# Performance work log

Hardware: AMD Instinct MI355X
Metric: run time of the kernel (lower is better)

The kernel has to match this reference:

```python
import jax, jax.numpy as jnp
import numpy as np

N = 100000
E = 1600000
IN_DIM = 128
HID = 64
EPS = 1e-5


def setup_inputs() -> dict:
    key = jax.random.key(0)
    ks = jax.random.split(key, 16)
    inp = {
        "x": jax.random.normal(ks[0], (N, IN_DIM), dtype=jnp.float32),
        "edge_index": jax.random.randint(ks[1], (2, E), 0, N, dtype=jnp.int64),
    }
    dims = [(HID, IN_DIM), (HID, HID), (HID, HID)]
    for i, (o, c) in enumerate(dims):
        inp[f"W{i}"] = jax.random.normal(ks[2 + 4 * i], (o, c), dtype=jnp.float32) / np.sqrt(c)
        inp[f"b{i}"] = jnp.zeros((o,), dtype=jnp.float32)
        inp[f"g{i}"] = jnp.ones((o,), dtype=jnp.float32)
        inp[f"be{i}"] = jnp.zeros((o,), dtype=jnp.float32)
    return inp


def _gcn_layer(x, W, b, src, dst, norm):
    # PyG GCNConv: linear first, then normalized sum aggregation, then bias
    h = x @ W.T                                  # [N, out]
    msg = h[src] * norm[:, None]                 # [E+N, out] gather (memory-bound)
    agg = jax.ops.segment_sum(msg, dst, num_segments=N)
    return agg + b


def _batchnorm(h, g, be):
    mean = jnp.mean(h, axis=0)
    var = jnp.mean((h - mean) ** 2, axis=0)      # biased var (training-mode BN)
    return (h - mean) * jax.lax.rsqrt(var + EPS) * g + be


def reference(x, edge_index, W0, b0, g0, be0, W1, b1, g1, be1, W2, b2, g2, be2):
    # add self loops (GCNConv default)
    loops = jnp.arange(N, dtype=edge_index.dtype)
    src = jnp.concatenate([edge_index[0], loops])
    dst = jnp.concatenate([edge_index[1], loops])
    # symmetric normalization: deg^{-1/2}[src] * deg^{-1/2}[dst]
    deg = jax.ops.segment_sum(jnp.ones_like(dst, dtype=x.dtype), dst, num_segments=N)
    dis = jax.lax.rsqrt(jnp.maximum(deg, 1.0))
    norm = dis[src] * dis[dst]

    params = [(W0, b0, g0, be0), (W1, b1, g1, be1), (W2, b2, g2, be2)]
    for W, b, g, be in params:
        h = _gcn_layer(x, W, b, src, dst, norm)
        h = _batchnorm(h, g, be)
        h = jax.nn.relu(h)
        x = x + h if h.shape == x.shape else h   # residual from layer 2 on
    return x
```

## Files before the change

### kernel.cpp

```cpp
#include <hip/hip_runtime.h>
#include <math.h>

#define NN 100000
#define NE 1600000
#define EPS_BN 1e-5f
#define NB 1000
#define BSZ 100
#define PCHUNK 8192

__device__ __forceinline__ unsigned bf16r(float x) {
  unsigned u = __float_as_uint(x);
  return (u + 0x7FFFu + ((u >> 16) & 1u)) >> 16;
}
__device__ __forceinline__ float bf16lo(unsigned w) { return __uint_as_float(w << 16); }
__device__ __forceinline__ float bf16hi(unsigned w) { return __uint_as_float(w & 0xFFFF0000u); }

__global__ void detect_kernel(const int* __restrict__ ei32, int* __restrict__ flag) {
  __shared__ int red[256];
  int t = threadIdx.x;
  int acc = 0;
#pragma unroll
  for (int k = 0; k < 4; ++k) acc |= ei32[2 * (t * 4 + k) + 1];
  red[t] = acc;
  __syncthreads();
  for (int off = 128; off > 0; off >>= 1) {
    if (t < off) red[t] |= red[t + off];
    __syncthreads();
  }
  if (t == 0) *flag = (red[0] == 0) ? 1 : 0;
}

__device__ __forceinline__ int edge_at(const void* ei, long long idx, int is64) {
  if (is64) return (int)((const long long*)ei)[idx];
  return ((const int*)ei)[idx];
}

__global__ __launch_bounds__(256) void bhist_kernel(const void* __restrict__ ei,
                                                    const int* __restrict__ flag,
                                                    int* __restrict__ bucket_cnt) {
  __shared__ int h[NB];
  int is64 = *flag;
  int t = threadIdx.x;
  for (int k = t; k < NB; k += 256) h[k] = 0;
  __syncthreads();
  for (int e = blockIdx.x * 256 + t; e < NE; e += gridDim.x * 256) {
    int d = edge_at(ei, (long long)NE + e, is64);
    atomicAdd(&h[d / BSZ], 1);
  }
  __syncthreads();
  for (int k = t; k < NB; k += 256) {
    int v = h[k];
    if (v) atomicAdd(&bucket_cnt[k], v);
  }
}

__global__ __launch_bounds__(1024) void bscan_kernel(const int* __restrict__ bucket_cnt,
                                                     int* __restrict__ bucket_base,
                                                     int* __restrict__ bucket_put,
                                                     int* __restrict__ row_start) {
  __shared__ int sh[1024];
  int t = threadIdx.x;
  int v = (t < NB) ? bucket_cnt[t] : 0;
  sh[t] = v;
  __syncthreads();
  for (int off = 1; off < 1024; off <<= 1) {
    int u = (t >= off) ? sh[t - off] : 0;
    __syncthreads();
    sh[t] += u;
    __syncthreads();
  }
  if (t < NB) {
    int b = sh[t] - v;
    bucket_base[t] = b;
    bucket_put[t] = b;
  }
  if (t == 0) row_start[NN] = NE;
}

__global__ __launch_bounds__(256) void bplace_kernel(const void* __restrict__ ei,
                                                     const int* __restrict__ flag,
                                                     int* __restrict__ bucket_put,
                                                     unsigned* __restrict__ staging) {
  __shared__ int hist[NB];
  __shared__ int base[NB];
  int is64 = *flag;
  int t = threadIdx.x;
  long long e0 = (long long)blockIdx.x * PCHUNK;
  int n = (int)min((long long)PCHUNK, (long long)NE - e0);
  for (int k = t; k < NB; k += 256) hist[k] = 0;
  __syncthreads();
  for (int k = t; k < n; k += 256) {
    int d = edge_at(ei, (long long)NE + e0 + k, is64);
    atomicAdd(&hist[d / BSZ], 1);
  }
  __syncthreads();
  for (int k = t; k < NB; k += 256) {
    int c = hist[k];
    base[k] = c ? atomicAdd(&bucket_put[k], c) : 0;
    hist[k] = 0;
  }
  __syncthreads();
  for (int k = t; k < n; k += 256) {
    int s = edge_at(ei, e0 + k, is64);
    int d = edge_at(ei, (long long)NE + e0 + k, is64);
    int b = d / BSZ;
    int p = base[b] + atomicAdd(&hist[b], 1);
    staging[p] = ((unsigned)s << 7) | (unsigned)(d - b * BSZ);
  }
}

__global__ __launch_bounds__(256) void bbuild_kernel(const unsigned* __restrict__ staging,
                                                     const int* __restrict__ bucket_base,
                                                     const int* __restrict__ bucket_cnt,
                                                     int* __restrict__ row_start,
                                                     float* __restrict__ dis,
                                                     int* __restrict__ csr_src) {
  __shared__ int deg[BSZ];
  __shared__ int excl[128];
  __shared__ int cur[BSZ];
  int b = blockIdx.x;
  int t = threadIdx.x;
  int base = bucket_base[b], cnt = bucket_cnt[b];
  for (int k = t; k < BSZ; k += 256) {
    deg[k] = 0;
    cur[k] = 0;
  }
  __syncthreads();
  for (int e = t; e < cnt; e += 256) {
    unsigned w = staging[base + e];
    atomicAdd(&deg[w & 127], 1);
  }
  __syncthreads();
  if (t < 128) excl[t] = (t < BSZ) ? deg[t] : 0;
  __syncthreads();
  for (int off = 1; off < 128; off <<= 1) {
    int u = 0;
    if (t < 128 && t >= off) u = excl[t - off];
    __syncthreads();
    if (t < 128) excl[t] += u;
    __syncthreads();
  }
  if (t < BSZ) {
    int ex = excl[t] - deg[t];
    row_start[b * BSZ + t] = base + ex;
    dis[b * BSZ + t] = rsqrtf((float)(deg[t] + 1));
    excl[t] = ex;
  }
  __syncthreads();
  for (int e = t; e < cnt; e += 256) {
    unsigned w = staging[base + e];
    int dl = w & 127;
    int p = base + excl[dl] + atomicAdd(&cur[dl], 1);
    csr_src[p] = (int)(w >> 7);
  }
}

__device__ __forceinline__ void bn_prologue(const float* __restrict__ stats,
                                            const float* __restrict__ g,
                                            const float* __restrict__ be, float* scb,
                                            float* shb, int t) {
  if (t < 64) {
    float m = stats[t] / (float)NN;
    float v = stats[64 + t] / (float)NN - m * m;
    float sc = g[t] * rsqrtf(fmaxf(v, 0.f) + EPS_BN);
    scb[t] = sc;
    shb[t] = be[t] - m * sc;
  }
}

template <int K>
__global__ __launch_bounds__(256) void gemm_kernel(const float* __restrict__ x,
                                                   const float* __restrict__ Wm,
                                                   const float* __restrict__ dis,
                                                   unsigned* __restrict__ h16) {
  constexpr int KC = K / 4;
  __shared__ float4 ws4[64 * KC];
  __shared__ float4 xs4[64 * KC];
  int t = threadIdx.x;
  int row0 = blockIdx.x * 64;
  const float4* W4 = (const float4*)Wm;
  for (int idx = t; idx < 64 * KC; idx += 256) {
    int j = idx / KC, kc = idx % KC;
    ws4[j * KC + (kc ^ (j & 7))] = W4[idx];
  }
  const float4* x4 = (const float4*)x;
  for (int idx = t; idx < 64 * KC; idx += 256) {
    int r = idx / KC, kc = idx % KC;
    int row = row0 + r;
    float4 v = make_float4(0.f, 0.f, 0.f, 0.f);
    if (row < NN) v = x4[(size_t)row * KC + kc];
    xs4[r * KC + kc] = v;
  }
  __syncthreads();
  int j = t & 63, wv = t >> 6;
  float acc[16];
#pragma unroll
  for (int r = 0; r < 16; ++r) acc[r] = 0.f;
  for (int kc = 0; kc < KC; ++kc) {
    float4 w = ws4[j * KC + (kc ^ (j & 7))];
#pragma unroll
    for (int r = 0; r < 16; ++r) {
      float4 xv = xs4[(wv * 16 + r) * KC + kc];
      acc[r] += w.x * xv.x + w.y * xv.y + w.z * xv.z + w.w * xv.w;
    }
  }
#pragma unroll
  for (int r = 0; r < 16; ++r) {
    int row = row0 + wv * 16 + r;
    float di = (row < NN) ? dis[row] : 0.f;
    float a = acc[r] * di;
    float part = __shfl_xor(a, 1, 64);
    if (row < NN && !(j & 1)) {
      h16[(size_t)row * 32 + (j >> 1)] = bf16r(a) | (bf16r(part) << 16);
    }
  }
}

template <bool RES>
__global__ __launch_bounds__(256) void gemmF_kernel(
    const float4* __restrict__ aggp, const float* __restrict__ stats,
    const float* __restrict__ g, const float* __restrict__ be,
    const float4* __restrict__ xres, float4* __restrict__ xout,
    const float* __restrict__ Wm, const float* __restrict__ dis,
    unsigned* __restrict__ h16) {
  constexpr int KC = 16;
  __shared__ float4 ws4[64 * KC];
  __shared__ float4 xs4[64 * KC];
  __shared__ float scb[64], shb[64];
  int t = threadIdx.x;
  int row0 = blockIdx.x * 64;
  bn_prologue(stats, g, be, scb, shb, t);
  const float4* W4 = (const float4*)Wm;
  for (int idx = t; idx < 64 * KC; idx += 256) {
    int j = idx / KC, kc = idx % KC;
    ws4[j * KC + (kc ^ (j & 7))] = W4[idx];
  }
  __syncthreads();
  for (int idx = t; idx < 64 * KC; idx += 256) {
    int r = idx / KC, kc = idx % KC;
    int row = row0 + r;
    float4 y = make_float4(0.f, 0.f, 0.f, 0.f);
    if (row < NN) {
      float4 a = aggp[(size_t)row * KC + kc];
      int f = kc * 4;
      y.x = fmaxf(fmaf(a.x, scb[f], shb[f]), 0.f);
      y.y = fmaxf(fmaf(a.y, scb[f + 1], shb[f + 1]), 0.f);
      y.z = fmaxf(fmaf(a.z, scb[f + 2], shb[f + 2]), 0.f);
      y.w = fmaxf(fmaf(a.w, scb[f + 3], shb[f + 3]), 0.f);
      if (RES) {
        float4 xr = xres[(size_t)row * KC + kc];
        y.x += xr.x;
        y.y += xr.y;
        y.z += xr.z;
        y.w += xr.w;
      }
      xout[(size_t)row * KC + kc] = y;
    }
    xs4[r * KC + kc] = y;
  }
  __syncthreads();
  int j = t & 63, wv = t >> 6;
  float acc[16];
#pragma unroll
  for (int r = 0; r < 16; ++r) acc[r] = 0.f;
  for (int kc = 0; kc < KC; ++kc) {
    float4 w = ws4[j * KC + (kc ^ (j & 7))];
#pragma unroll
    for (int r = 0; r < 16; ++r) {
      float4 xv = xs4[(wv * 16 + r) * KC + kc];
      acc[r] += w.x * xv.x + w.y * xv.y + w.z * xv.z + w.w * xv.w;
    }
  }
#pragma unroll
  for (int r = 0; r < 16; ++r) {
    int row = row0 + wv * 16 + r;
    float di = (row < NN) ? dis[row] : 0.f;
    float a = acc[r] * di;
    float part = __shfl_xor(a, 1, 64);
    if (row < NN && !(j & 1)) {
      h16[(size_t)row * 32 + (j >> 1)] = bf16r(a) | (bf16r(part) << 16);
    }
  }
}

__global__ __launch_bounds__(256) void agg_kernel(const unsigned* __restrict__ h16,
                                                  const int* __restrict__ row_start,
                                                  const int* __restrict__ csr_src,
                                                  const float* __restrict__ dis,
                                                  float4* __restrict__ agg4,
                                                  float* __restrict__ stats) {
  const uint2* h2 = (const uint2*)h16;
  int t = threadIdx.x, lane = t & 63, wv = t >> 6;
  int c = lane & 15;
  int g = lane >> 4;
  int gw = blockIdx.x * 4 + wv;
  int nw = gridDim.x * 4;
  float s0 = 0.f, s1 = 0.f, s2 = 0.f, s3 = 0.f;
  float q0 = 0.f, q1 = 0.f, q2 = 0.f, q3 = 0.f;
  for (int i0 = gw; i0 < NN; i0 += nw) {
    int i = __builtin_amdgcn_readfirstlane(i0);
    int beg = row_start[i], end = row_start[i + 1];
    float di = dis[i];
    uint2 ws = h2[(size_t)i * 16 + c];
    float sw = (g == 0) ? 1.f : 0.f;
    float a0 = bf16lo(ws.x) * sw, a1 = bf16hi(ws.x) * sw;
    float a2 = bf16lo(ws.y) * sw, a3 = bf16hi(ws.y) * sw;
    int e = beg;
    for (; e + 8 <= end; e += 8) {
      int r0 = csr_src[e], r1 = csr_src[e + 1], r2 = csr_src[e + 2], r3 = csr_src[e + 3];
      int r4 = csr_src[e + 4], r5 = csr_src[e + 5], r6 = csr_src[e + 6], r7 = csr_src[e + 7];
      int ra = (g == 0) ? r0 : (g == 1) ? r1 : (g == 2) ? r2 : r3;
      int rb = (g == 0) ? r4 : (g == 1) ? r5 : (g == 2) ? r6 : r7;
      uint2 wa = h2[(size_t)ra * 16 + c];
      uint2 wb = h2[(size_t)rb * 16 + c];
      a0 += bf16lo(wa.x);
      a1 += bf16hi(wa.x);
      a2 += bf16lo(wa.y);
      a3 += bf16hi(wa.y);
      a0 += bf16lo(wb.x);
      a1 += bf16hi(wb.x);
      a2 += bf16lo(wb.y);
      a3 += bf16hi(wb.y);
    }
    if (e + 4 <= end) {
      int r0 = csr_src[e], r1 = csr_src[e + 1], r2 = csr_src[e + 2], r3 = csr_src[e + 3];
      int ra = (g == 0) ? r0 : (g == 1) ? r1 : (g == 2) ? r2 : r3;
      uint2 wa = h2[(size_t)ra * 16 + c];
      a0 += bf16lo(wa.x);
      a1 += bf16hi(wa.x);
      a2 += bf16lo(wa.y);
      a3 += bf16hi(wa.y);
      e += 4;
    }
    if (e < end) {
      int last = end - 1;
      int r0 = csr_src[e];
      int r1 = csr_src[min(e + 1, last)];
      int r2 = csr_src[min(e + 2, last)];
      int r3 = csr_src[min(e + 3, last)];
      int ra = (g == 0) ? r0 : (g == 1) ? r1 : (g == 2) ? r2 : r3;
      float wt = (e + g < end) ? 1.f : 0.f;
      uint2 wa = h2[(size_t)ra * 16 + c];
      a0 += bf16lo(wa.x) * wt;
      a1 += bf16hi(wa.x) * wt;
      a2 += bf16lo(wa.y) * wt;
      a3 += bf16hi(wa.y) * wt;
    }
#pragma unroll
    for (int m = 16; m <= 32; m <<= 1) {
      a0 += __shfl_xor(a0, m, 64);
      a1 += __shfl_xor(a1, m, 64);
      a2 += __shfl_xor(a2, m, 64);
      a3 += __shfl_xor(a3, m, 64);
    }
    a0 *= di;
    a1 *= di;
    a2 *= di;
    a3 *= di;
    if (lane < 16) {
      agg4[(size_t)i * 16 + c] = make_float4(a0, a1, a2, a3);
      s0 += a0;
      s1 += a1;
      s2 += a2;
      s3 += a3;
      q0 += a0 * a0;
      q1 += a1 * a1;
      q2 += a2 * a2;
      q3 += a3 * a3;
    }
  }
  __shared__ float redS[4][64];
  __shared__ float redQ[4][64];
  if (lane < 16) {
    redS[wv][4 * c + 0] = s0;
    redS[wv][4 * c + 1] = s1;
    redS[wv][4 * c + 2] = s2;
    redS[wv][4 * c + 3] = s3;
    redQ[wv][4 * c + 0] = q0;
    redQ[wv][4 * c + 1] = q1;
    redQ[wv][4 * c + 2] = q2;
    redQ[wv][4 * c + 3] = q3;
  }
  __syncthreads();
  if (wv == 0) {
    float a = redS[0][lane] + redS[1][lane] + redS[2][lane] + redS[3][lane];
    float b = redQ[0][lane] + redQ[1][lane] + redQ[2][lane] + redQ[3][lane];
    atomicAdd(&stats[lane], a);
    atomicAdd(&stats[64 + lane], b);
  }
}

__global__ __launch_bounds__(256) void applyF_kernel(const float* __restrict__ agg,
                                                     const float* __restrict__ stats,
                                                     const float* __restrict__ g,
                                                     const float* __restrict__ be,
                                                     const float* __restrict__ xres,
                                                     float* __restrict__ out) {
  __shared__ float scb[64], shb[64];
  int t = threadIdx.x;
  bn_prologue(stats, g, be, scb, shb, t);
  __syncthreads();
  const int total4 = NN * 16;
  for (int i = blockIdx.x * blockDim.x + t; i < total4; i += gridDim.x * blockDim.x) {
    float4 a = ((const float4*)agg)[i];
    int f = (i * 4) & 63;
    float4 y;
    y.x = fmaxf(fmaf(a.x, scb[f], shb[f]), 0.f);
    y.y = fmaxf(fmaf(a.y, scb[f + 1], shb[f + 1]), 0.f);
    y.z = fmaxf(fmaf(a.z, scb[f + 2], shb[f + 2]), 0.f);
    y.w = fmaxf(fmaf(a.w, scb[f + 3], shb[f + 3]), 0.f);
    float4 xr = ((const float4*)xres)[i];
    y.x += xr.x;
    y.y += xr.y;
    y.z += xr.z;
    y.w += xr.w;
    ((float4*)out)[i] = y;
  }
}

extern "C" void kernel_launch(void* const* d_in, const int* in_sizes, int n_in,
                              void* d_out, int out_size, void* d_ws, size_t ws_size,
                              hipStream_t stream) {
  const float* x0 = (const float*)d_in[0];
  const void* ei = d_in[1];
  const float* W0 = (const float*)d_in[2];
  const float* g0 = (const float*)d_in[4];
  const float* be0 = (const float*)d_in[5];
  const float* W1 = (const float*)d_in[6];
  const float* g1 = (const float*)d_in[8];
  const float* be1 = (const float*)d_in[9];
  const float* W2 = (const float*)d_in[10];
  const float* g2 = (const float*)d_in[12];
  const float* be2 = (const float*)d_in[13];
  float* out = (float*)d_out;

  char* p = (char*)d_ws;
  auto carve = [&](size_t bytes) {
    char* q = p;
    p += (bytes + 255) & ~(size_t)255;
    return (void*)q;
  };
  float* bufA = (float*)carve((size_t)NN * 64 * 4);
  unsigned* h16 = (unsigned*)carve((size_t)NN * 32 * 4);
  float* bufC = (float*)carve((size_t)NN * 64 * 4);
  int* row_start = (int*)carve((size_t)(NN + 1) * 4);
  float* dis = (float*)carve((size_t)NN * 4);
  int* csr_src = (int*)carve((size_t)NE * 4);
  unsigned* staging = (unsigned*)carve((size_t)NE * 4);
  int* bucket_cnt = (int*)carve(NB * 4);
  int* bucket_base = (int*)carve(NB * 4);
  int* bucket_put = (int*)carve(NB * 4);
  float* stats0 = (float*)carve(128 * 4);
  float* stats1 = (float*)carve(128 * 4);
  float* stats2 = (float*)carve(128 * 4);
  int* flag = (int*)carve(256);

  detect_kernel<<<1, 256, 0, stream>>>((const int*)ei, flag);
  hipMemsetAsync(bucket_cnt, 0, NB * 4, stream);
  hipMemsetAsync(stats0, 0, 3 * 128 * 4, stream);
  bhist_kernel<<<256, 256, 0, stream>>>(ei, flag, bucket_cnt);
  bscan_kernel<<<1, 1024, 0, stream>>>(bucket_cnt, bucket_base, bucket_put, row_start);
  const int place_blocks = (NE + PCHUNK - 1) / PCHUNK;
  bplace_kernel<<<place_blocks, 256, 0, stream>>>(ei, flag, bucket_put, staging);
  bbuild_kernel<<<NB, 256, 0, stream>>>(staging, bucket_base, bucket_cnt, row_start, dis,
                                        csr_src);

  const int gemm_blocks = (NN + 63) / 64;

  gemm_kernel<128><<<gemm_blocks, 256, 0, stream>>>(x0, W0, dis, h16);
  agg_kernel<<<2048, 256, 0, stream>>>(h16, row_start, csr_src, dis, (float4*)bufC,
                                       stats0);

  gemmF_kernel<false><<<gemm_blocks, 256, 0, stream>>>(
      (const float4*)bufC, stats0, g0, be0, nullptr, (float4*)bufA, W1, dis, h16);
  agg_kernel<<<2048, 256, 0, stream>>>(h16, row_start, csr_src, dis, (float4*)bufC,
                                       stats1);

  gemmF_kernel<true><<<gemm_blocks, 256, 0, stream>>>(
      (const float4*)bufC, stats1, g1, be1, (const float4*)bufA, (float4*)out, W2, dis,
      h16);
  agg_kernel<<<2048, 256, 0, stream>>>(h16, row_start, csr_src, dis, (float4*)bufC,
                                       stats2);

  applyF_kernel<<<1024, 256, 0, stream>>>(bufC, stats2, g2, be2, out, out);
}
```

Measured before the change: 444.3 us.

## Split bf16 feature table into two 32-column slices for aggregation

The GEMM kernels now write h16 as two feature slices, each a contiguous [N,16-word] array, instead of one interleaved 64-column row. The aggregation kernel gives each block one slice (chosen by block parity), so a wavefront handles 8 neighbours at once with 64-byte rows and uses a wider shuffle reduction. Each slice table is half the size, which should improve cache hit rates for the random gathers. In exchange, every CSR edge list is read twice, the grid is halved per slice, and the per-node instruction count grows because of the 8-way select.

Measured after the change: 480.7 us. +8.2%, slower.

```diff
diff --git a/kernel.cpp b/kernel.cpp
--- a/kernel.cpp
+++ b/kernel.cpp
@@ -168,6 +168,10 @@
   }
 }
 
+__device__ __forceinline__ size_t hword(int sl, int row, int w15) {
+  return (size_t)sl * (NN * 16) + (size_t)row * 16 + w15;
+}
+
 template <int K>
 __global__ __launch_bounds__(256) void gemm_kernel(const float* __restrict__ x,
                                                    const float* __restrict__ Wm,
@@ -211,7 +215,8 @@
     float a = acc[r] * di;
     float part = __shfl_xor(a, 1, 64);
     if (row < NN && !(j & 1)) {
-      h16[(size_t)row * 32 + (j >> 1)] = bf16r(a) | (bf16r(part) << 16);
+      int w = j >> 1;
+      h16[hword(w >> 4, row, w & 15)] = bf16r(a) | (bf16r(part) << 16);
     }
   }
 }
@@ -278,7 +283,8 @@
     float a = acc[r] * di;
     float part = __shfl_xor(a, 1, 64);
     if (row < NN && !(j & 1)) {
-      h16[(size_t)row * 32 + (j >> 1)] = bf16r(a) | (bf16r(part) << 16);
+      int w = j >> 1;
+      h16[hword(w >> 4, row, w & 15)] = bf16r(a) | (bf16r(part) << 16);
     }
   }
 }
@@ -289,30 +295,44 @@
                                                   const float* __restrict__ dis,
                                                   float4* __restrict__ agg4,
                                                   float* __restrict__ stats) {
-  const uint2* h2 = (const uint2*)h16;
   int t = threadIdx.x, lane = t & 63, wv = t >> 6;
-  int c = lane & 15;
-  int g = lane >> 4;
-  int gw = blockIdx.x * 4 + wv;
-  int nw = gridDim.x * 4;
+  int sl = blockIdx.x & 1;
+  const uint2* h2 = (const uint2*)h16 + (size_t)sl * (NN * 8);
+  int c = lane & 7;
+  int g = lane >> 3;
+  int gw = (blockIdx.x >> 1) * 4 + wv;
+  int nw = (gridDim.x >> 1) * 4;
   float s0 = 0.f, s1 = 0.f, s2 = 0.f, s3 = 0.f;
   float q0 = 0.f, q1 = 0.f, q2 = 0.f, q3 = 0.f;
   for (int i0 = gw; i0 < NN; i0 += nw) {
     int i = __builtin_amdgcn_readfirstlane(i0);
     int beg = row_start[i], end = row_start[i + 1];
     float di = dis[i];
-    uint2 ws = h2[(size_t)i * 16 + c];
+    uint2 ws = h2[(size_t)i * 8 + c];
     float sw = (g == 0) ? 1.f : 0.f;
     float a0 = bf16lo(ws.x) * sw, a1 = bf16hi(ws.x) * sw;
     float a2 = bf16lo(ws.y) * sw, a3 = bf16hi(ws.y) * sw;
     int e = beg;
-    for (; e + 8 <= end; e += 8) {
-      int r0 = csr_src[e], r1 = csr_src[e + 1], r2 = csr_src[e + 2], r3 = csr_src[e + 3];
-      int r4 = csr_src[e + 4], r5 = csr_src[e + 5], r6 = csr_src[e + 6], r7 = csr_src[e + 7];
-      int ra = (g == 0) ? r0 : (g == 1) ? r1 : (g == 2) ? r2 : r3;
-      int rb = (g == 0) ? r4 : (g == 1) ? r5 : (g == 2) ? r6 : r7;
-      uint2 wa = h2[(size_t)ra * 16 + c];
-      uint2 wb = h2[(size_t)rb * 16 + c];
+#define SEL8(base_e)                                                               \
+  ({                                                                               \
+    int r0 = csr_src[(base_e)], r1 = csr_src[(base_e) + 1],                        \
+        r2 = csr_src[(base_e) + 2], r3 = csr_src[(base_e) + 3],                    \
+        r4 = csr_src[(base_e) + 4], r5 = csr_src[(base_e) + 5],                    \
+        r6 = csr_src[(base_e) + 6], r7 = csr_src[(base_e) + 7];                    \
+    (g == 0) ? r0                                                                  \
+             : (g == 1) ? r1                                                       \
+                        : (g == 2) ? r2                                            \
+                                   : (g == 3) ? r3                                 \
+                                              : (g == 4) ? r4                      \
+                                                         : (g == 5) ? r5           \
+                                                                    : (g == 6) ? r6\
+                                                                                : r7; \
+  })
+    for (; e + 16 <= end; e += 16) {
+      int ra = SEL8(e);
+      int rb = SEL8(e + 8);
+      uint2 wa = h2[(size_t)ra * 8 + c];
+      uint2 wb = h2[(size_t)rb * 8 + c];
       a0 += bf16lo(wa.x);
       a1 += bf16hi(wa.x);
       a2 += bf16lo(wa.y);
@@ -322,15 +342,14 @@
       a2 += bf16lo(wb.y);
       a3 += bf16hi(wb.y);
     }
-    if (e + 4 <= end) {
-      int r0 = csr_src[e], r1 = csr_src[e + 1], r2 = csr_src[e + 2], r3 = csr_src[e + 3];
-      int ra = (g == 0) ? r0 : (g == 1) ? r1 : (g == 2) ? r2 : r3;
-      uint2 wa = h2[(size_t)ra * 16 + c];
+    if (e + 8 <= end) {
+      int ra = SEL8(e);
+      uint2 wa = h2[(size_t)ra * 8 + c];
       a0 += bf16lo(wa.x);
       a1 += bf16hi(wa.x);
       a2 += bf16lo(wa.y);
       a3 += bf16hi(wa.y);
-      e += 4;
+      e += 8;
     }
     if (e < end) {
       int last = end - 1;
@@ -338,16 +357,27 @@
       int r1 = csr_src[min(e + 1, last)];
       int r2 = csr_src[min(e + 2, last)];
       int r3 = csr_src[min(e + 3, last)];
-      int ra = (g == 0) ? r0 : (g == 1) ? r1 : (g == 2) ? r2 : r3;
+      int r4 = csr_src[min(e + 4, last)];
+      int r5 = csr_src[min(e + 5, last)];
+      int r6 = csr_src[min(e + 6, last)];
+      int r7 = csr_src[min(e + 7, last)];
+      int ra = (g == 0) ? r0
+                        : (g == 1) ? r1
+                                   : (g == 2) ? r2
+                                              : (g == 3) ? r3
+                                                         : (g == 4) ? r4
+                                                                    : (g == 5) ? r5
+                                                                               : (g == 6) ? r6 : r7;
       float wt = (e + g < end) ? 1.f : 0.f;
-      uint2 wa = h2[(size_t)ra * 16 + c];
+      uint2 wa = h2[(size_t)ra * 8 + c];
       a0 += bf16lo(wa.x) * wt;
       a1 += bf16hi(wa.x) * wt;
       a2 += bf16lo(wa.y) * wt;
       a3 += bf16hi(wa.y) * wt;
     }
-#pragma unroll
-    for (int m = 16; m <= 32; m <<= 1) {
+#undef SEL8
+#pragma unroll
+    for (int m = 8; m <= 32; m <<= 1) {
       a0 += __shfl_xor(a0, m, 64);
       a1 += __shfl_xor(a1, m, 64);
       a2 += __shfl_xor(a2, m, 64);
@@ -357,8 +387,8 @@
     a1 *= di;
     a2 *= di;
     a3 *= di;
-    if (lane < 16) {
-      agg4[(size_t)i * 16 + c] = make_float4(a0, a1, a2, a3);
+    if (lane < 8) {
+      agg4[(size_t)i * 16 + sl * 8 + c] = make_float4(a0, a1, a2, a3);
       s0 += a0;
       s1 += a1;
       s2 += a2;
@@ -369,9 +399,9 @@
       q3 += a3 * a3;
     }
   }
-  __shared__ float redS[4][64];
-  __shared__ float redQ[4][64];
-  if (lane < 16) {
+  __shared__ float redS[4][32];
+  __shared__ float redQ[4][32];
+  if (lane < 8) {
     redS[wv][4 * c + 0] = s0;
     redS[wv][4 * c + 1] = s1;
     redS[wv][4 * c + 2] = s2;
@@ -382,11 +412,11 @@
     redQ[wv][4 * c + 3] = q3;
   }
   __syncthreads();
-  if (wv == 0) {
+  if (wv == 0 && lane < 32) {
     float a = redS[0][lane] + redS[1][lane] + redS[2][lane] + redS[3][lane];
     float b = redQ[0][lane] + redQ[1][lane] + redQ[2][lane] + redQ[3][lane];
-    atomicAdd(&stats[lane], a);
-    atomicAdd(&stats[64 + lane], b);
+    atomicAdd(&stats[sl * 32 + lane], a);
+    atomicAdd(&stats[64 + sl * 32 + lane], b);
   }
 }
 
```
